# Kernel optimization log

Hardware: AMD Instinct MI355X
Metric: run time of the kernel (lower is better)

Reference implementation:

```python
import jax, jax.numpy as jnp
import numpy as np

B, E, XD = 2, 196608, 128     # batch, num edges (fine nodes), per-edge node feature dim
EIN, EOUT = 4, 128            # edge embedder dims
NREC = 12288                  # receiver (coarse) node count = 12*32^2
LIN, LOUT = EOUT + XD, 256    # output FFN dims


def setup_inputs() -> dict:
    key = jax.random.key(0)
    ks = jax.random.split(key, 8)
    w = lambda k, sh: jax.random.normal(k, sh, jnp.float32) * 0.05
    return {
        "x": jax.random.normal(ks[0], (B, E, XD), jnp.float32),
        "edge_attr": jax.random.normal(ks[1], (E, EIN), jnp.float32),
        "edge_index": jax.random.randint(ks[2], (2, E), 0, NREC, jnp.int32),
        # edge_embedder MLP: Linear(EIN,EOUT) -> SiLU -> Linear(EOUT,EOUT)
        "W1": w(ks[3], (EIN, EOUT)), "b1": jnp.zeros((EOUT,), jnp.float32),
        "W2": w(ks[4], (EOUT, EOUT)), "b2": jnp.zeros((EOUT,), jnp.float32),
        # output FeedForward: Linear(LIN,LOUT) -> SiLU -> Linear(LOUT,LOUT)
        "L1": w(ks[5], (LIN, LOUT)), "c1": jnp.zeros((LOUT,), jnp.float32),
        "L2": w(ks[6], (LOUT, LOUT)), "c2": jnp.zeros((LOUT,), jnp.float32),
    }


def reference(x, edge_attr, edge_index, W1, b1, W2, b2, L1, c1, L2, c2):
    # Edge MLP embed: [E, EIN] -> [E, EOUT]
    h = jax.nn.silu(edge_attr @ W1 + b1) @ W2 + b2
    # Broadcast edge features over batch and concat with per-edge node features
    ef = jnp.broadcast_to(h[None], (x.shape[0], h.shape[0], h.shape[1]))
    v = jnp.concatenate([ef, x], axis=-1)                 # [B, E, EOUT+XD]
    recv = edge_index[1]                                  # [E] in [0, NREC)
    # scatter_sum over edges -> receiver nodes, per batch
    agg = jax.vmap(lambda vb: jax.ops.segment_sum(vb, recv, num_segments=NREC))(v)  # [B, NREC, LIN]
    # Output FFN
    return jax.nn.silu(agg @ L1 + c1) @ L2 + c2           # [B, NREC, LOUT]
```

## Files before the change

kernel.cpp:

```cpp
#include <hip/hip_runtime.h>
#include <hip/hip_bf16.h>
#include <cstdint>
#include <cstddef>

#define B_     2
#define E_     196608
#define XD_    128
#define NREC_  12288
#define EOUT_  128
#define LIN_   256
#define LOUT_  256
#define M_     (B_ * NREC_)

typedef __attribute__((ext_vector_type(8))) short short8;
typedef __attribute__((ext_vector_type(4))) float f32x4;

__device__ __forceinline__ unsigned short f2bf(float f) {
    union { float f; unsigned u; } v; v.f = f;
    unsigned r = v.u + 0x7FFFu + ((v.u >> 16) & 1u);
    return (unsigned short)(r >> 16);
}

__global__ __launch_bounds__(256) void precompute(
        const float* __restrict__ W2, const float* __restrict__ b2,
        const float* __restrict__ L1, const float* __restrict__ L2,
        unsigned short* __restrict__ L1T, unsigned short* __restrict__ L2T,
        float* __restrict__ v) {
    int bid = blockIdx.x;
    int n = threadIdx.x;
    if (bid < 128) {
        int j = bid;
        float a0 = 0.f, a1 = 0.f, a2 = 0.f, a3 = 0.f;
        for (int c = 0; c < 128; c += 4) {
            a0 = fmaf(W2[j * 128 + c + 0], L1[(c + 0) * 256 + n], a0);
            a1 = fmaf(W2[j * 128 + c + 1], L1[(c + 1) * 256 + n], a1);
            a2 = fmaf(W2[j * 128 + c + 2], L1[(c + 2) * 256 + n], a2);
            a3 = fmaf(W2[j * 128 + c + 3], L1[(c + 3) * 256 + n], a3);
        }
        L1T[n * 256 + j] = f2bf((a0 + a1) + (a2 + a3));
        if (j == 0) {
            float s0 = 0.f, s1 = 0.f;
            for (int c = 0; c < 128; c += 2) {
                s0 = fmaf(b2[c + 0], L1[(c + 0) * 256 + n], s0);
                s1 = fmaf(b2[c + 1], L1[(c + 1) * 256 + n], s1);
            }
            v[n] = s0 + s1;
        }
    } else if (bid < 256) {
        int k = bid;
        L1T[n * 256 + k] = f2bf(L1[k * 256 + n]);
    } else {
        int k = bid - 256;
        L2T[n * 256 + k] = f2bf(L2[k * 256 + n]);
    }
}

__global__ __launch_bounds__(256) void count_kernel(const int* __restrict__ recv,
                                                    int* __restrict__ cnt) {
    int e = blockIdx.x * 256 + threadIdx.x;
    if (e < E_) atomicAdd(&cnt[recv[e]], 1);
}

__global__ __launch_bounds__(1024) void scan_kernel(const int* __restrict__ cnt,
                                                    int* __restrict__ rowStart,
                                                    int* __restrict__ cursor) {
    __shared__ int sums[1024];
    int tid = threadIdx.x;
    int base = tid * 12;
    int local[12];
    int s = 0;
    #pragma unroll
    for (int j = 0; j < 12; ++j) { local[j] = s; s += cnt[base + j]; }
    sums[tid] = s;
    __syncthreads();
    for (int off = 1; off < 1024; off <<= 1) {
        int vv = sums[tid];
        int add = (tid >= off) ? sums[tid - off] : 0;
        __syncthreads();
        sums[tid] = vv + add;
        __syncthreads();
    }
    int excl = (tid == 0) ? 0 : sums[tid - 1];
    #pragma unroll
    for (int j = 0; j < 12; ++j) {
        int vv = excl + local[j];
        rowStart[base + j] = vv;
        cursor[base + j] = vv;
    }
    if (tid == 1023) rowStart[NREC_] = excl + s;
}

__global__ __launch_bounds__(256) void fill_kernel(const int* __restrict__ recv,
                                                   int* __restrict__ cursor,
                                                   int* __restrict__ edge_ids) {
    int e = blockIdx.x * 256 + threadIdx.x;
    if (e < E_) {
        int p = atomicAdd(&cursor[recv[e]], 1);
        edge_ids[p] = e;
    }
}

__global__ __launch_bounds__(128) void gather_kernel(
        const float* __restrict__ x, const float* __restrict__ ea,
        const float* __restrict__ W1, const float* __restrict__ b1,
        const int* __restrict__ rowStart, const int* __restrict__ edge_ids,
        unsigned short* __restrict__ agg_bf) {
    int r = blockIdx.x;
    int c = threadIdx.x;
    int k0 = __builtin_amdgcn_readfirstlane(rowStart[r]);
    int k1 = __builtin_amdgcn_readfirstlane(rowStart[r + 1]);
    float w10 = W1[c], w11 = W1[128 + c], w12 = W1[256 + c], w13 = W1[384 + c];
    float bb1 = b1[c];
    const float* xb = x + (size_t)E_ * 128;
    float accS = 0.f, aX0 = 0.f, aX1 = 0.f;
    int k = k0;
    for (; k + 8 <= k1; k += 8) {
        int e[8];
        #pragma unroll
        for (int u = 0; u < 8; ++u)
            e[u] = __builtin_amdgcn_readfirstlane(edge_ids[k + u]);
        float xa[8], xc[8];
        float4 q[8];
        #pragma unroll
        for (int u = 0; u < 8; ++u) {
            xa[u] = x[(size_t)e[u] * 128 + c];
            xc[u] = xb[(size_t)e[u] * 128 + c];
            q[u] = *(const float4*)(ea + (size_t)e[u] * 4);
        }
        #pragma unroll
        for (int u = 0; u < 8; ++u) {
            float p = fmaf(q[u].x, w10, fmaf(q[u].y, w11,
                      fmaf(q[u].z, w12, fmaf(q[u].w, w13, bb1))));
            accS += p / (1.f + __expf(-p));
            aX0 += xa[u];
            aX1 += xc[u];
        }
    }
    for (; k < k1; ++k) {
        int e0 = __builtin_amdgcn_readfirstlane(edge_ids[k]);
        float4 q = *(const float4*)(ea + (size_t)e0 * 4);
        float p = fmaf(q.x, w10, fmaf(q.y, w11, fmaf(q.z, w12, fmaf(q.w, w13, bb1))));
        accS += p / (1.f + __expf(-p));
        aX0 += x[(size_t)e0 * 128 + c];
        aX1 += xb[(size_t)e0 * 128 + c];
    }
    unsigned short sb = f2bf(accS);
    agg_bf[(size_t)r * 256 + c] = sb;
    agg_bf[(size_t)(NREC_ + r) * 256 + c] = sb;
    agg_bf[(size_t)r * 256 + 128 + c] = f2bf(aX0);
    agg_bf[(size_t)(NREC_ + r) * 256 + 128 + c] = f2bf(aX1);
}

__global__ __launch_bounds__(256) void ffn_kernel(
        const unsigned short* __restrict__ agg,
        const unsigned short* __restrict__ L1T, const float* __restrict__ c1,
        const unsigned short* __restrict__ L2T, const float* __restrict__ c2,
        const float* __restrict__ v, const int* __restrict__ cnt,
        float* __restrict__ out) {
    __shared__ unsigned short T[64][264];
    int tid  = threadIdx.x;
    int wave = tid >> 6;
    int lane = tid & 63;
    int quad = lane >> 4;
    int l16  = lane & 15;
    int m0 = blockIdx.x * 64 + wave * 16;

    float cntv[4];
    #pragma unroll
    for (int rr = 0; rr < 4; ++rr) {
        int m = m0 + quad * 4 + rr;
        int r = (m >= NREC_) ? m - NREC_ : m;
        cntv[rr] = (float)cnt[r];
    }

    short8 afrag[8];
    const unsigned short* aptr = agg + (size_t)(m0 + l16) * 256 + quad * 8;
    #pragma unroll
    for (int ks = 0; ks < 8; ++ks)
        afrag[ks] = *(const short8*)(aptr + ks * 32);

    #pragma unroll 2
    for (int nt = 0; nt < 16; ++nt) {
        f32x4 acc = {0.f, 0.f, 0.f, 0.f};
        const unsigned short* bptr = L1T + (size_t)(nt * 16 + l16) * 256 + quad * 8;
        #pragma unroll
        for (int ks = 0; ks < 8; ++ks) {
            short8 bfrag = *(const short8*)(bptr + ks * 32);
            acc = __builtin_amdgcn_mfma_f32_16x16x32_bf16(afrag[ks], bfrag, acc, 0, 0, 0);
        }
        #pragma unroll
        for (int rr = 0; rr < 4; ++rr) {
            int row = quad * 4 + rr;
            int col = nt * 16 + l16;
            float pv = acc[rr] + c1[col] + cntv[rr] * v[col];
            pv = pv / (1.f + __expf(-pv));
            T[wave * 16 + row][col] = f2bf(pv);
        }
    }
    __syncthreads();

    short8 afrag2[8];
    #pragma unroll
    for (int ks = 0; ks < 8; ++ks)
        afrag2[ks] = *(const short8*)&T[wave * 16 + l16][ks * 32 + quad * 8];

    #pragma unroll 2
    for (int nt = 0; nt < 16; ++nt) {
        f32x4 acc = {0.f, 0.f, 0.f, 0.f};
        const unsigned short* bptr = L2T + (size_t)(nt * 16 + l16) * 256 + quad * 8;
        #pragma unroll
        for (int ks = 0; ks < 8; ++ks) {
            short8 bfrag = *(const short8*)(bptr + ks * 32);
            acc = __builtin_amdgcn_mfma_f32_16x16x32_bf16(afrag2[ks], bfrag, acc, 0, 0, 0);
        }
        #pragma unroll
        for (int rr = 0; rr < 4; ++rr) {
            int row = m0 + quad * 4 + rr;
            int col = nt * 16 + l16;
            out[(size_t)row * 256 + col] = acc[rr] + c2[col];
        }
    }
}

extern "C" void kernel_launch(void* const* d_in, const int* in_sizes, int n_in,
                              void* d_out, int out_size, void* d_ws, size_t ws_size,
                              hipStream_t stream) {
    const float* x          = (const float*)d_in[0];
    const float* edge_attr  = (const float*)d_in[1];
    const int*   edge_index = (const int*)d_in[2];
    const float* W1 = (const float*)d_in[3];
    const float* b1 = (const float*)d_in[4];
    const float* W2 = (const float*)d_in[5];
    const float* b2 = (const float*)d_in[6];
    const float* L1 = (const float*)d_in[7];
    const float* c1 = (const float*)d_in[8];
    const float* L2 = (const float*)d_in[9];
    const float* c2 = (const float*)d_in[10];
    float* out = (float*)d_out;

    int* cnt      = (int*)d_ws;
    int* rowStart = cnt + NREC_;
    int* cursor   = rowStart + NREC_ + 4;
    int* edge_ids = cursor + NREC_;
    unsigned short* agg_bf = (unsigned short*)(edge_ids + E_);
    unsigned short* L1T = agg_bf + (size_t)M_ * 256;
    unsigned short* L2T = L1T + 256 * 256;
    float* v = (float*)(L2T + 256 * 256);

    const int* recv = edge_index + E_;

    hipMemsetAsync(cnt, 0, NREC_ * sizeof(int), stream);
    precompute<<<512, 256, 0, stream>>>(W2, b2, L1, L2, L1T, L2T, v);
    count_kernel<<<(E_ + 255) / 256, 256, 0, stream>>>(recv, cnt);
    scan_kernel<<<1, 1024, 0, stream>>>(cnt, rowStart, cursor);
    fill_kernel<<<(E_ + 255) / 256, 256, 0, stream>>>(recv, cursor, edge_ids);
    gather_kernel<<<NREC_, 128, 0, stream>>>(x, edge_attr, W1, b1,
                                             rowStart, edge_ids, agg_bf);
    ffn_kernel<<<M_ / 64, 256, 0, stream>>>(agg_bf, L1T, c1, L2T, c2, v, cnt, out);
}
```

Baseline: 412.0 us.

## Vectorize gather x loads as float4 with edge-split waves and LDS reduction

Rewrites the gather kernel so each lane loads 16-byte float4 chunks of x: the two waves split edges (even/odd), and lanes cover both batches × 32 column chunks. The partial sums are then reduced through shared memory and written as packed bf16. Edges are processed in masked groups of 16 instead of 8 plus a scalar tail. The aim is wider, fewer memory transactions and more loads in flight. In exchange it adds a barrier, LDS traffic, and wasted SiLU work on padded edges for receivers with few edges.

```diff
diff --git a/kernel.cpp b/kernel.cpp
--- a/kernel.cpp
+++ b/kernel.cpp
@@ -105,50 +105,70 @@
         const float* __restrict__ W1, const float* __restrict__ b1,
         const int* __restrict__ rowStart, const int* __restrict__ edge_ids,
         unsigned short* __restrict__ agg_bf) {
+    __shared__ f32x4 xred[128];
     int r = blockIdx.x;
-    int c = threadIdx.x;
+    int t = threadIdx.x;
     int k0 = __builtin_amdgcn_readfirstlane(rowStart[r]);
     int k1 = __builtin_amdgcn_readfirstlane(rowStart[r + 1]);
-    float w10 = W1[c], w11 = W1[128 + c], w12 = W1[256 + c], w13 = W1[384 + c];
-    float bb1 = b1[c];
-    const float* xb = x + (size_t)E_ * 128;
-    float accS = 0.f, aX0 = 0.f, aX1 = 0.f;
-    int k = k0;
-    for (; k + 8 <= k1; k += 8) {
-        int e[8];
-        #pragma unroll
-        for (int u = 0; u < 8; ++u)
-            e[u] = __builtin_amdgcn_readfirstlane(edge_ids[k + u]);
-        float xa[8], xc[8];
-        float4 q[8];
-        #pragma unroll
-        for (int u = 0; u < 8; ++u) {
-            xa[u] = x[(size_t)e[u] * 128 + c];
-            xc[u] = xb[(size_t)e[u] * 128 + c];
-            q[u] = *(const float4*)(ea + (size_t)e[u] * 4);
-        }
-        #pragma unroll
-        for (int u = 0; u < 8; ++u) {
-            float p = fmaf(q[u].x, w10, fmaf(q[u].y, w11,
-                      fmaf(q[u].z, w12, fmaf(q[u].w, w13, bb1))));
-            accS += p / (1.f + __expf(-p));
-            aX0 += xa[u];
-            aX1 += xc[u];
-        }
-    }
-    for (; k < k1; ++k) {
-        int e0 = __builtin_amdgcn_readfirstlane(edge_ids[k]);
-        float4 q = *(const float4*)(ea + (size_t)e0 * 4);
-        float p = fmaf(q.x, w10, fmaf(q.y, w11, fmaf(q.z, w12, fmaf(q.w, w13, bb1))));
-        accS += p / (1.f + __expf(-p));
-        aX0 += x[(size_t)e0 * 128 + c];
-        aX1 += xb[(size_t)e0 * 128 + c];
-    }
+
+    float w10 = W1[t], w11 = W1[128 + t], w12 = W1[256 + t], w13 = W1[384 + t];
+    float bb1 = b1[t];
+    float accS = 0.f;
+
+    int p  = t >> 6;
+    int s  = t & 63;
+    int b  = s >> 5;
+    int c4 = s & 31;
+    const float* xbase = x + (size_t)b * E_ * 128 + c4 * 4;
+    f32x4 aX = {0.f, 0.f, 0.f, 0.f};
+
+    for (int k = k0; k < k1; k += 16) {
+        int ecnt = k1 - k;
+        int eid[16];
+        #pragma unroll
+        for (int u = 0; u < 16; ++u) {
+            int idx = k + u;
+            idx = (idx < k1) ? idx : (k1 - 1);
+            eid[u] = __builtin_amdgcn_readfirstlane(edge_ids[idx]);
+        }
+        f32x4 xv[8];
+        #pragma unroll
+        for (int i = 0; i < 8; ++i)
+            xv[i] = *(const f32x4*)(xbase + (size_t)eid[2 * i + p] * 128);
+        #pragma unroll
+        for (int u = 0; u < 16; ++u) {
+            float4 q = *(const float4*)(ea + (size_t)eid[u] * 4);
+            float pr = fmaf(q.x, w10, fmaf(q.y, w11,
+                       fmaf(q.z, w12, fmaf(q.w, w13, bb1))));
+            float sv = pr / (1.f + __expf(-pr));
+            accS += (u < ecnt) ? sv : 0.f;
+        }
+        #pragma unroll
+        for (int i = 0; i < 8; ++i) {
+            float m = ((2 * i + p) < ecnt) ? 1.f : 0.f;
+            aX[0] = fmaf(m, xv[i][0], aX[0]);
+            aX[1] = fmaf(m, xv[i][1], aX[1]);
+            aX[2] = fmaf(m, xv[i][2], aX[2]);
+            aX[3] = fmaf(m, xv[i][3], aX[3]);
+        }
+    }
+
+    xred[t] = aX;
     unsigned short sb = f2bf(accS);
-    agg_bf[(size_t)r * 256 + c] = sb;
-    agg_bf[(size_t)(NREC_ + r) * 256 + c] = sb;
-    agg_bf[(size_t)r * 256 + 128 + c] = f2bf(aX0);
-    agg_bf[(size_t)(NREC_ + r) * 256 + 128 + c] = f2bf(aX1);
+    agg_bf[(size_t)r * 256 + t] = sb;
+    agg_bf[(size_t)(NREC_ + r) * 256 + t] = sb;
+    __syncthreads();
+    if (t < 64) {
+        f32x4 v0 = xred[t];
+        f32x4 v1 = xred[t + 64];
+        float t0 = v0[0] + v1[0], t1 = v0[1] + v1[1];
+        float t2 = v0[2] + v1[2], t3 = v0[3] + v1[3];
+        unsigned lo = (unsigned)f2bf(t0) | ((unsigned)f2bf(t1) << 16);
+        unsigned hi = (unsigned)f2bf(t2) | ((unsigned)f2bf(t3) << 16);
+        uint2 pk = make_uint2(lo, hi);
+        int bb = t >> 5, cc = t & 31;
+        *(uint2*)(agg_bf + ((size_t)(bb * NREC_ + r) * 256 + 128 + cc * 4)) = pk;
+    }
 }
 
 __global__ __launch_bounds__(256) void ffn_kernel(
```

Result: no change. 414.8 us (+0.7%).

## Assign one wavefront per receiver row with float4 x loads in gather

Applied to the files above, without the earlier changes.

The gather kernel now maps one 64-lane wavefront to each receiver row instead of a 128-thread block. Lanes read both batches' x rows with 16-byte vector loads, and each lane computes two SiLU-edge channels. The scalar tail loop is replaced by a masked final 8-edge chunk whose indices are clamped to the last valid edge. The goal is fewer, wider memory instructions and less per-edge instruction overhead, paid for with redundant masked work in the final chunk of each row.

```diff
diff --git a/kernel.cpp b/kernel.cpp
--- a/kernel.cpp
+++ b/kernel.cpp
@@ -100,55 +100,76 @@
     }
 }
 
-__global__ __launch_bounds__(128) void gather_kernel(
+__global__ __launch_bounds__(256) void gather_kernel(
         const float* __restrict__ x, const float* __restrict__ ea,
         const float* __restrict__ W1, const float* __restrict__ b1,
         const int* __restrict__ rowStart, const int* __restrict__ edge_ids,
         unsigned short* __restrict__ agg_bf) {
-    int r = blockIdx.x;
-    int c = threadIdx.x;
+    int wave = threadIdx.x >> 6;
+    int lane = threadIdx.x & 63;
+    int r = blockIdx.x * 4 + wave;
     int k0 = __builtin_amdgcn_readfirstlane(rowStart[r]);
     int k1 = __builtin_amdgcn_readfirstlane(rowStart[r + 1]);
-    float w10 = W1[c], w11 = W1[128 + c], w12 = W1[256 + c], w13 = W1[384 + c];
-    float bb1 = b1[c];
-    const float* xb = x + (size_t)E_ * 128;
-    float accS = 0.f, aX0 = 0.f, aX1 = 0.f;
-    int k = k0;
-    for (; k + 8 <= k1; k += 8) {
-        int e[8];
+
+    int c = lane;
+    float w0a = W1[c],       w1a = W1[128 + c];
+    float w2a = W1[256 + c], w3a = W1[384 + c];
+    float w0b = W1[c + 64],  w1b = W1[192 + c];
+    float w2b = W1[320 + c], w3b = W1[448 + c];
+    float ba = b1[c], bb = b1[c + 64];
+    float accA = 0.f, accB = 0.f;
+
+    int b  = lane >> 5;
+    int c4 = lane & 31;
+    const float* xbase = x + (size_t)b * ((size_t)E_ * 128) + c4 * 4;
+    f32x4 aX = {0.f, 0.f, 0.f, 0.f};
+
+    for (int k = k0; k < k1; k += 8) {
+        int eid[8];
+        #pragma unroll
+        for (int u = 0; u < 8; ++u) {
+            int idx = k + u;
+            idx = (idx < k1) ? idx : (k1 - 1);
+            eid[u] = __builtin_amdgcn_readfirstlane(edge_ids[idx]);
+        }
+        f32x4 xv[8];
         #pragma unroll
         for (int u = 0; u < 8; ++u)
-            e[u] = __builtin_amdgcn_readfirstlane(edge_ids[k + u]);
-        float xa[8], xc[8];
-        float4 q[8];
+            xv[u] = *(const f32x4*)(xbase + (size_t)eid[u] * 128);
         #pragma unroll
         for (int u = 0; u < 8; ++u) {
-            xa[u] = x[(size_t)e[u] * 128 + c];
-            xc[u] = xb[(size_t)e[u] * 128 + c];
-            q[u] = *(const float4*)(ea + (size_t)e[u] * 4);
+            float4 q = *(const float4*)(ea + (size_t)eid[u] * 4);
+            float pa = fmaf(q.x, w0a, fmaf(q.y, w1a,
+                       fmaf(q.z, w2a, fmaf(q.w, w3a, ba))));
+            float pb = fmaf(q.x, w0b, fmaf(q.y, w1b,
+                       fmaf(q.z, w2b, fmaf(q.w, w3b, bb))));
+            float sa = pa / (1.f + __expf(-pa));
+            float sb = pb / (1.f + __expf(-pb));
+            bool live = (k + u) < k1;
+            accA += live ? sa : 0.f;
+            accB += live ? sb : 0.f;
         }
         #pragma unroll
         for (int u = 0; u < 8; ++u) {
-            float p = fmaf(q[u].x, w10, fmaf(q[u].y, w11,
-                      fmaf(q[u].z, w12, fmaf(q[u].w, w13, bb1))));
-            accS += p / (1.f + __expf(-p));
-            aX0 += xa[u];
-            aX1 += xc[u];
-        }
-    }
-    for (; k < k1; ++k) {
-        int e0 = __builtin_amdgcn_readfirstlane(edge_ids[k]);
-        float4 q = *(const float4*)(ea + (size_t)e0 * 4);
-        float p = fmaf(q.x, w10, fmaf(q.y, w11, fmaf(q.z, w12, fmaf(q.w, w13, bb1))));
-        accS += p / (1.f + __expf(-p));
-        aX0 += x[(size_t)e0 * 128 + c];
-        aX1 += xb[(size_t)e0 * 128 + c];
-    }
-    unsigned short sb = f2bf(accS);
-    agg_bf[(size_t)r * 256 + c] = sb;
-    agg_bf[(size_t)(NREC_ + r) * 256 + c] = sb;
-    agg_bf[(size_t)r * 256 + 128 + c] = f2bf(aX0);
-    agg_bf[(size_t)(NREC_ + r) * 256 + 128 + c] = f2bf(aX1);
+            float m = ((k + u) < k1) ? 1.f : 0.f;
+            aX[0] = fmaf(m, xv[u][0], aX[0]);
+            aX[1] = fmaf(m, xv[u][1], aX[1]);
+            aX[2] = fmaf(m, xv[u][2], aX[2]);
+            aX[3] = fmaf(m, xv[u][3], aX[3]);
+        }
+    }
+
+    unsigned short sa16 = f2bf(accA), sb16 = f2bf(accB);
+    size_t base0 = (size_t)r * 256;
+    size_t base1 = (size_t)(NREC_ + r) * 256;
+    agg_bf[base0 + c] = sa16;
+    agg_bf[base0 + c + 64] = sb16;
+    agg_bf[base1 + c] = sa16;
+    agg_bf[base1 + c + 64] = sb16;
+    unsigned lo = (unsigned)f2bf(aX[0]) | ((unsigned)f2bf(aX[1]) << 16);
+    unsigned hi = (unsigned)f2bf(aX[2]) | ((unsigned)f2bf(aX[3]) << 16);
+    *(uint2*)(agg_bf + (size_t)(b * NREC_ + r) * 256 + 128 + c4 * 4) =
+        make_uint2(lo, hi);
 }
 
 __global__ __launch_bounds__(256) void ffn_kernel(
@@ -254,7 +275,7 @@
     count_kernel<<<(E_ + 255) / 256, 256, 0, stream>>>(recv, cnt);
     scan_kernel<<<1, 1024, 0, stream>>>(cnt, rowStart, cursor);
     fill_kernel<<<(E_ + 255) / 256, 256, 0, stream>>>(recv, cursor, edge_ids);
-    gather_kernel<<<NREC_, 128, 0, stream>>>(x, edge_attr, W1, b1,
-                                             rowStart, edge_ids, agg_bf);
+    gather_kernel<<<NREC_ / 4, 256, 0, stream>>>(x, edge_attr, W1, b1,
+                                                 rowStart, edge_ids, agg_bf);
     ffn_kernel<<<M_ / 64, 256, 0, stream>>>(agg_bf, L1T, c1, L2T, c2, v, cnt, out);
 }
```

New measurement: 412.5 us. No clear change (+0.1%).
